# Performance work log

Hardware: AMD Instinct MI355X
Metric: run time of the kernel (lower is better)

Reference implementation:

```python
import jax, jax.numpy as jnp
import numpy as np

T, N, F_IN, H1, H2, F_OUT = 48, 4096, 64, 64, 32, 64

def setup_inputs() -> dict:
    key = jax.random.key(0)
    ks = jax.random.split(key, 14)
    sc = 0.05
    x = jax.random.normal(ks[0], (T, N, F_IN), jnp.float32)
    adj = jax.random.uniform(ks[1], (N, N), jnp.float32) / N  # roughly row-normalized dense adjacency
    fc_w = jax.random.normal(ks[2], (F_IN, H1), jnp.float32) * sc
    fc_b = jnp.zeros((H1,), jnp.float32)
    Wz = jax.random.normal(ks[3], (H1, F_OUT), jnp.float32) * sc
    Wr = jax.random.normal(ks[4], (H1, F_OUT), jnp.float32) * sc
    Wh = jax.random.normal(ks[5], (H1, F_OUT), jnp.float32) * sc
    Lz = jax.random.normal(ks[6], (2 * F_OUT, F_OUT), jnp.float32) * sc
    Lr = jax.random.normal(ks[7], (2 * F_OUT, F_OUT), jnp.float32) * sc
    Lh = jax.random.normal(ks[8], (2 * F_OUT, F_OUT), jnp.float32) * sc
    bz = jnp.zeros((F_OUT,), jnp.float32)
    br = jnp.zeros((F_OUT,), jnp.float32)
    bh = jnp.zeros((F_OUT,), jnp.float32)
    return {"x": x, "adj": adj, "fc_w": fc_w, "fc_b": fc_b,
            "Wz": Wz, "Wr": Wr, "Wh": Wh,
            "Lz": Lz, "Lr": Lr, "Lh": Lh,
            "bz": bz, "br": br, "bh": bh}

def reference(x, adj, fc_w, fc_b, Wz, Wr, Wh, Lz, Lr, Lh, bz, br, bh):
    # relu(fc(x)) followed by relu(unsqueeze) == single relu
    xh = jax.nn.relu(x @ fc_w + fc_b)          # [T, N, H1]
    h0 = jnp.zeros((N, F_OUT), x.dtype)

    def step(h, xi):
        # TGCN cell: dense graph conv A @ (X W) feeding GRU-style gates
        az = adj @ (xi @ Wz)                   # [N, F_OUT]
        ar = adj @ (xi @ Wr)
        ah = adj @ (xi @ Wh)
        z = jax.nn.sigmoid(jnp.concatenate([az, h], axis=-1) @ Lz + bz)
        r = jax.nn.sigmoid(jnp.concatenate([ar, h], axis=-1) @ Lr + br)
        h_tilde = jnp.tanh(jnp.concatenate([ah, h * r], axis=-1) @ Lh + bh)
        h_new = z * h + (1.0 - z) * h_tilde
        return h_new, None

    h, _ = jax.lax.scan(step, h0, xh)
    return h[None]                              # [1, N, F_OUT]
```

## Files before the change

kernel.cpp:

```cpp
#include <hip/hip_runtime.h>

typedef unsigned short u16;
typedef unsigned char u8;
typedef short s16x8 __attribute__((ext_vector_type(8)));
typedef unsigned short u16x4 __attribute__((ext_vector_type(4)));
typedef float f32x4 __attribute__((ext_vector_type(4)));
typedef int i32x4 __attribute__((ext_vector_type(4)));
typedef int i32x8 __attribute__((ext_vector_type(8)));

#define AS1 __attribute__((address_space(1)))
#define AS3 __attribute__((address_space(3)))

__device__ __forceinline__ void g2l16(const void* g, void* l) {
  __builtin_amdgcn_global_load_lds((const AS1 void*)g, (AS3 void*)l, 16, 0, 0);
}

__device__ __forceinline__ float b2f(u16 u) {
  union { unsigned int i; float f; } x; x.i = ((unsigned int)u) << 16; return x.f;
}
__device__ __forceinline__ u16 f2b(float f) {
  unsigned int u = __builtin_bit_cast(unsigned int, f);
  return (u16)((u + 0x7fffu + ((u >> 16) & 1u)) >> 16);
}
__device__ __forceinline__ u8 f2e4m3(float v) {
  int p = __builtin_amdgcn_cvt_pk_fp8_f32(v, 0.f, 0, false);
  return (u8)(p & 0xff);
}
__device__ __forceinline__ float sigm(float x) { return 1.f / (1.f + __expf(-x)); }
__device__ __forceinline__ float tanh_f(float x) { return 2.f / (1.f + __expf(-2.f * x)) - 1.f; }


__global__ __launch_bounds__(256) void kpre(
    const float* __restrict__ a, u8* __restrict__ ab,
    const float* __restrict__ fcw, const float* __restrict__ fcb,
    const float* __restrict__ x, u8* __restrict__ xht,
    const float* __restrict__ Wz, const float* __restrict__ Wr, const float* __restrict__ Wh,
    const float* __restrict__ Lz, const float* __restrict__ Lr, const float* __restrict__ Lh,
    u16* __restrict__ wct, u16* __restrict__ lbt) {
  int b = blockIdx.x, tid = threadIdx.x;
  if (b < 4096) {
    size_t idx = (size_t)b * 256 + tid;
    const float4* src = (const float4*)a;
    unsigned int* dst = (unsigned int*)ab;
#pragma unroll
    for (int k = 0; k < 4; ++k) {
      size_t f = idx + (size_t)k * 1048576;
      float4 v = src[f];
      unsigned int p = __builtin_amdgcn_cvt_pk_fp8_f32(v.x * 4096.f, v.y * 4096.f, 0, false);
      p = __builtin_amdgcn_cvt_pk_fp8_f32(v.z * 4096.f, v.w * 4096.f, p, true);
      int row = (int)(f >> 10);
      int col0 = ((int)f & 1023) << 2;
      unsigned int dstb = (unsigned int)(((row >> 7) * 32 + (col0 >> 7)) << 14) +
                          (((row >> 4) & 7) << 11) +
                          (((row & 15) | (((col0 >> 5) & 3) << 4)) << 5) + (col0 & 31);
      dst[dstb >> 2] = p;
    }
    return;
  }
  if (b < 4144) {
    int idx = (b - 4096) * 256 + tid;
    int c_cat = idx >> 6, hh = idx & 63;
    int g = c_cat >> 6, c = c_cat & 63;
    const float* W = (g == 0) ? Wz : (g == 1) ? Wr : Wh;
    const float* L = (g == 0) ? Lz : (g == 1) ? Lr : Lh;
    float acc = 0.f;
    for (int m = 0; m < 64; ++m) acc += W[hh * 64 + m] * L[m * 64 + c];
    wct[c_cat * 64 + hh] = f2b(acc);
    return;
  }
  if (b < 4147) {
    int g = b - 4144;
    const float* L = (g == 0) ? Lz : (g == 1) ? Lr : Lh;
    for (int i = 0; i < 16; ++i) {
      int idx = tid * 16 + i; int c = idx >> 6, hh = idx & 63;
      lbt[g * 4096 + c * 64 + hh] = f2b(L[(64 + hh) * 64 + c]);
    }
    return;
  }
  int kb = b - 4147;
  int t = kb >> 5, n0 = (kb & 31) * 128;
  __shared__ __align__(16) u16 xs[128 * 72];
  __shared__ __align__(16) u16 fw[64 * 72];
  __shared__ __align__(16) u8 xh8[64 * 128];
  __shared__ float fb[64];
  int w = tid >> 6, l = tid & 63;
#pragma unroll
  for (int i = 0; i < 16; ++i) {
    int idx = tid + i * 256;
    int h = idx & 63, f = idx >> 6;
    fw[h * 72 + f] = f2b(fcw[f * 64 + h]);
  }
  const float4* xg = (const float4*)(x + ((size_t)t * 4096 + n0) * 64);
#pragma unroll
  for (int i = 0; i < 8; ++i) {
    int f = tid + i * 256;
    float4 v = xg[f];
    u16x4 p; p[0] = f2b(v.x); p[1] = f2b(v.y); p[2] = f2b(v.z); p[3] = f2b(v.w);
    *(u16x4*)&xs[(f >> 4) * 72 + (f & 15) * 4] = p;
  }
  if (tid < 64) fb[tid] = fcb[tid];
  __syncthreads();

  int lm = l & 15, q = l >> 4;
  f32x4 acc[4][2];
#pragma unroll
  for (int i = 0; i < 4; ++i)
#pragma unroll
    for (int j = 0; j < 2; ++j)
#pragma unroll
      for (int r = 0; r < 4; ++r) acc[i][j][r] = 0.f;
#pragma unroll
  for (int s = 0; s < 2; ++s) {
    s16x8 af[4], bf[2];
#pragma unroll
    for (int i = 0; i < 4; ++i) af[i] = *(const s16x8*)&fw[(16 * i + lm) * 72 + 32 * s + q * 8];
#pragma unroll
    for (int j = 0; j < 2; ++j) bf[j] = *(const s16x8*)&xs[(32 * w + 16 * j + lm) * 72 + 32 * s + q * 8];
#pragma unroll
    for (int i = 0; i < 4; ++i)
#pragma unroll
      for (int j = 0; j < 2; ++j)
        acc[i][j] = __builtin_amdgcn_mfma_f32_16x16x32_bf16(af[i], bf[j], acc[i][j], 0, 0, 0);
  }
#pragma unroll
  for (int i = 0; i < 4; ++i)
#pragma unroll
    for (int j = 0; j < 2; ++j) {
      int node = 32 * w + 16 * j + lm;
      int h0 = 16 * i + q * 4;
#pragma unroll
      for (int r = 0; r < 4; ++r) {
        float v = acc[i][j][r] + fb[h0 + r];
        xh8[(h0 + r) * 128 + node] = f2e4m3(v > 0.f ? v : 0.f);
      }
    }
  __syncthreads();
  {
    int h = tid >> 2, seg = tid & 3;
    u8* dst = xht + (size_t)(t * 64 + h) * 4096 + n0 + seg * 32;
    const u8* src = &xh8[h * 128 + seg * 32];
    *(i32x4*)dst = *(const i32x4*)src;
    *(i32x4*)(dst + 16) = *(const i32x4*)(src + 16);
  }
}

__global__ __launch_bounds__(256) void k2(
    const u8* __restrict__ A, const u8* __restrict__ B, u16* __restrict__ M) {
  __shared__ __align__(16) u8 sh[49152];
  int tid = threadIdx.x, w = tid >> 6, l = tid & 63;
  int nt = blockIdx.x, mt = blockIdx.y;
  const u8* Bb = B + (size_t)nt * 192 * 4096;
  int lm = l & 15, q = l >> 4;
  int wm = w >> 1, wn = w & 1;
  int srow = l >> 3, scol = l & 7;
  const u8* At = A + (size_t)mt * 32 * 16384 + (size_t)(4 * wm) * 2048 + (size_t)l * 32;
  f32x4 acc[4][6];
#pragma unroll
  for (int i = 0; i < 4; ++i)
#pragma unroll
    for (int j = 0; j < 6; ++j)
#pragma unroll
      for (int r = 0; r < 4; ++r) acc[i][j][r] = 0.f;

#define STAGE_B(bsel, kk)                                                     \
  do {                                                                        \
    u8* Bs_ = sh + (bsel) * 24576;                                            \
    _Pragma("unroll") for (int j = 0; j < 6; ++j) {      \
      int r0 = 48 * w + 8 * j;                                                \
      int row = r0 + srow;                                                    \
      int c = (scol - row) & 7;                                               \
      g2l16(Bb + (size_t)row * 4096 + (kk) + c * 16, Bs_ + r0 * 128);         \
    }                                                                         \
  } while (0)

  STAGE_B(0, 0);
  __syncthreads();

  for (int it = 0; it < 32; ++it) {
    int cur = it & 1;
    i32x8 a8[4];
#pragma unroll
    for (int i = 0; i < 4; ++i)
      a8[i] = *(const i32x8*)(At + (size_t)it * 16384 + i * 2048);
    if (it < 31) STAGE_B(cur ^ 1, (it + 1) * 128);
    const u8* Bs = sh + cur * 24576;
#pragma unroll
    for (int j = 0; j < 6; ++j) {
      int rb = 96 * wn + 16 * j + lm;
      int q0 = (2 * q + rb) & 7, q1 = (2 * q + 1 + rb) & 7;
      i32x4 lo2 = *(const i32x4*)&Bs[rb * 128 + q0 * 16];
      i32x4 hi2 = *(const i32x4*)&Bs[rb * 128 + q1 * 16];
      i32x8 b8 = __builtin_shufflevector(lo2, hi2, 0, 1, 2, 3, 4, 5, 6, 7);
#pragma unroll
      for (int i = 0; i < 4; ++i)
        acc[i][j] = __builtin_amdgcn_mfma_scale_f32_16x16x128_f8f6f4(
            a8[i], b8, acc[i][j], 0, 0, 0, 127, 0, 127);
    }
    __syncthreads();
  }
#undef STAGE_B

  u16* tb = (u16*)sh;
  const float sc = 1.f / 4096.f;
#pragma unroll
  for (int p = 0; p < 2; ++p) {
    if (p) __syncthreads();
    if (wm == p) {
#pragma unroll
      for (int i = 0; i < 4; ++i)
#pragma unroll
        for (int j = 0; j < 6; ++j)
#pragma unroll
          for (int r = 0; r < 4; ++r)
            tb[(16 * i + 4 * q + r) * 200 + 96 * wn + 16 * j + lm] = f2b(acc[i][j][r] * sc);
    }
    __syncthreads();
    int row = tid >> 2, seg = tid & 3;
    u16* dst = M + (size_t)(mt * 128 + p * 64 + row) * 3072 + nt * 192 + seg * 48;
    const u16* src = &tb[row * 200 + seg * 48];
#pragma unroll
    for (int v = 0; v < 6; ++v)
      *(i32x4*)(dst + 8 * v) = *(const i32x4*)(src + 8 * v);
  }
}

__global__ __launch_bounds__(256) void k3(
    const u16* __restrict__ M, const u16* __restrict__ wct, const u16* __restrict__ lbt,
    const float* __restrict__ bz, const float* __restrict__ br, const float* __restrict__ bh,
    float* __restrict__ out) {
  __shared__ __align__(16) u16 hhi[1024], hlo[1024];
  __shared__ __align__(16) u16 rhi[1024], rlo[1024];
  int tid = threadIdx.x, w = tid >> 6, l = tid & 63;
  int nb0 = blockIdx.x * 16;
  int lm = l & 15, q = l >> 4;
  int am = lm & 7;
  int cb = 16 * w + q * 4;
  int rd0 = lm * 64 + ((q ^ am) * 8);
  int rd1 = lm * 64 + (((4 + q) ^ am) * 8);
  int wi  = lm * 64 + (((2 * w + (q >> 1)) ^ am) * 8) + 4 * (q & 1);
  s16x8 afw[3][2], afl[3][2];
#pragma unroll
  for (int g = 0; g < 3; ++g)
#pragma unroll
    for (int s = 0; s < 2; ++s) {
      afw[g][s] = *(const s16x8*)&wct[(size_t)(g * 64 + 16 * w + lm) * 64 + 32 * s + q * 8];
      afl[g][s] = *(const s16x8*)&lbt[(size_t)(g * 64 + 16 * w + lm) * 64 + 32 * s + q * 8];
    }
  for (int i = tid; i < 1024; i += 256) { hhi[i] = 0; hlo[i] = 0; }
  f32x4 bzv, brv, bhv, hv;
#pragma unroll
  for (int r = 0; r < 4; ++r) {
    bzv[r] = bz[cb + r]; brv[r] = br[cb + r]; bhv[r] = bh[cb + r]; hv[r] = 0.f;
  }
  const f32x4 zf = {0.f, 0.f, 0.f, 0.f};
  __syncthreads();

  const u16* Mrow = M + (size_t)(nb0 + lm) * 3072;
  s16x8 Mn[2];
  Mn[0] = *(const s16x8*)&Mrow[q * 8];
  Mn[1] = *(const s16x8*)&Mrow[32 + q * 8];
  f32x4 uzwC = __builtin_amdgcn_mfma_f32_16x16x32_bf16(afw[0][0], Mn[0], bzv, 0, 0, 0);
  uzwC = __builtin_amdgcn_mfma_f32_16x16x32_bf16(afw[0][1], Mn[1], uzwC, 0, 0, 0);
  f32x4 urwC = __builtin_amdgcn_mfma_f32_16x16x32_bf16(afw[1][0], Mn[0], brv, 0, 0, 0);
  urwC = __builtin_amdgcn_mfma_f32_16x16x32_bf16(afw[1][1], Mn[1], urwC, 0, 0, 0);
  f32x4 uhwC = __builtin_amdgcn_mfma_f32_16x16x32_bf16(afw[2][0], Mn[0], bhv, 0, 0, 0);
  uhwC = __builtin_amdgcn_mfma_f32_16x16x32_bf16(afw[2][1], Mn[1], uhwC, 0, 0, 0);

  for (int t = 0; t < 48; ++t) {
    if (t < 47) {
      Mn[0] = *(const s16x8*)&Mrow[(t + 1) * 64 + q * 8];
      Mn[1] = *(const s16x8*)&Mrow[(t + 1) * 64 + 32 + q * 8];
    }
    s16x8 hh0 = *(const s16x8*)&hhi[rd0], hh1 = *(const s16x8*)&hhi[rd1];
    s16x8 hl0 = *(const s16x8*)&hlo[rd0], hl1 = *(const s16x8*)&hlo[rd1];
    f32x4 uzA = __builtin_amdgcn_mfma_f32_16x16x32_bf16(afl[0][0], hh0, uzwC, 0, 0, 0);
    uzA = __builtin_amdgcn_mfma_f32_16x16x32_bf16(afl[0][1], hh1, uzA, 0, 0, 0);
    f32x4 uzB = __builtin_amdgcn_mfma_f32_16x16x32_bf16(afl[0][0], hl0, zf, 0, 0, 0);
    uzB = __builtin_amdgcn_mfma_f32_16x16x32_bf16(afl[0][1], hl1, uzB, 0, 0, 0);
    f32x4 urA = __builtin_amdgcn_mfma_f32_16x16x32_bf16(afl[1][0], hh0, urwC, 0, 0, 0);
    urA = __builtin_amdgcn_mfma_f32_16x16x32_bf16(afl[1][1], hh1, urA, 0, 0, 0);
    f32x4 urB = __builtin_amdgcn_mfma_f32_16x16x32_bf16(afl[1][0], hl0, zf, 0, 0, 0);
    urB = __builtin_amdgcn_mfma_f32_16x16x32_bf16(afl[1][1], hl1, urB, 0, 0, 0);
    f32x4 zv, rv;
#pragma unroll
    for (int r = 0; r < 4; ++r) {
      zv[r] = sigm(uzA[r] + uzB[r]);
      rv[r] = sigm(urA[r] + urB[r]);
    }
    {
      u16x4 phi, plo;
#pragma unroll
      for (int r = 0; r < 4; ++r) {
        float p = hv[r] * rv[r];
        u16 hi = f2b(p); phi[r] = hi; plo[r] = f2b(p - b2f(hi));
      }
      *(u16x4*)&rhi[wi] = phi;
      *(u16x4*)&rlo[wi] = plo;
    }
    __syncthreads();
    s16x8 rh0 = *(const s16x8*)&rhi[rd0], rh1 = *(const s16x8*)&rhi[rd1];
    s16x8 rl0 = *(const s16x8*)&rlo[rd0], rl1 = *(const s16x8*)&rlo[rd1];
    f32x4 uhA = __builtin_amdgcn_mfma_f32_16x16x32_bf16(afl[2][0], rh0, uhwC, 0, 0, 0);
    uhA = __builtin_amdgcn_mfma_f32_16x16x32_bf16(afl[2][1], rh1, uhA, 0, 0, 0);
    f32x4 uhB = __builtin_amdgcn_mfma_f32_16x16x32_bf16(afl[2][0], rl0, zf, 0, 0, 0);
    uhB = __builtin_amdgcn_mfma_f32_16x16x32_bf16(afl[2][1], rl1, uhB, 0, 0, 0);
    {
      u16x4 phi, plo;
#pragma unroll
      for (int r = 0; r < 4; ++r) {
        float th = tanh_f(uhA[r] + uhB[r]);
        float hn = zv[r] * hv[r] + (1.f - zv[r]) * th;
        hv[r] = hn;
        u16 hi = f2b(hn); phi[r] = hi; plo[r] = f2b(hn - b2f(hi));
      }
      *(u16x4*)&hhi[wi] = phi;
      *(u16x4*)&hlo[wi] = plo;
    }
    if (t < 47) {
      uzwC = __builtin_amdgcn_mfma_f32_16x16x32_bf16(afw[0][0], Mn[0], bzv, 0, 0, 0);
      uzwC = __builtin_amdgcn_mfma_f32_16x16x32_bf16(afw[0][1], Mn[1], uzwC, 0, 0, 0);
      urwC = __builtin_amdgcn_mfma_f32_16x16x32_bf16(afw[1][0], Mn[0], brv, 0, 0, 0);
      urwC = __builtin_amdgcn_mfma_f32_16x16x32_bf16(afw[1][1], Mn[1], urwC, 0, 0, 0);
      uhwC = __builtin_amdgcn_mfma_f32_16x16x32_bf16(afw[2][0], Mn[0], bhv, 0, 0, 0);
      uhwC = __builtin_amdgcn_mfma_f32_16x16x32_bf16(afw[2][1], Mn[1], uhwC, 0, 0, 0);
    }
    __syncthreads();
  }
#pragma unroll
  for (int r = 0; r < 4; ++r)
    out[(size_t)(nb0 + lm) * 64 + cb + r] = hv[r];
}

extern "C" void kernel_launch(void* const* d_in, const int* in_sizes, int n_in,
                              void* d_out, int out_size, void* d_ws, size_t ws_size,
                              hipStream_t stream) {
  const float* x   = (const float*)d_in[0];
  const float* adj = (const float*)d_in[1];
  const float* fcw = (const float*)d_in[2];
  const float* fcb = (const float*)d_in[3];
  const float* Wz  = (const float*)d_in[4];
  const float* Wr  = (const float*)d_in[5];
  const float* Wh  = (const float*)d_in[6];
  const float* Lz  = (const float*)d_in[7];
  const float* Lr  = (const float*)d_in[8];
  const float* Lh  = (const float*)d_in[9];
  const float* bz  = (const float*)d_in[10];
  const float* br  = (const float*)d_in[11];
  const float* bh  = (const float*)d_in[12];
  char* ws = (char*)d_ws;
  u8*  xht  = (u8*)(ws);
  u8*  adj8 = (u8*)(ws + (size_t)12582912);
  u16* Mm   = (u16*)(ws + (size_t)29360128);
  u16* wct  = (u16*)(ws + (size_t)54525952);
  u16* lbt  = (u16*)(ws + (size_t)54550528);
  float* outp = (float*)d_out;

  hipLaunchKernelGGL(kpre, dim3(5683), dim3(256), 0, stream,
                     adj, adj8, fcw, fcb, x, xht, Wz, Wr, Wh, Lz, Lr, Lh, wct, lbt);
  hipLaunchKernelGGL(k2, dim3(16, 32), dim3(256), 0, stream, adj8, xht, Mm);
  hipLaunchKernelGGL(k3, dim3(256), dim3(256), 0, stream, Mm, wct, lbt, bz, br, bh, outp);
}
```

Before: 257.8 us.

## Double k2 block to 512 threads and software-pipeline A/B loads with MFMA

The adjacency GEMM kernel now uses 512-thread blocks covering 256 rows, so each staged B tile in LDS is shared by twice as many waves, and the grid is halved. The main loop is manually unrolled by two with ping-pong A register buffers. B staging and the next A loads are interleaved between two halves of the MFMA work, using explicit vmcnt waits, raw barriers and s_setprio to overlap memory with matrix math. The cost is higher register pressure from the doubled A fragments, and the hand-placed waitcnt/barrier ordering is fragile.

```diff
diff --git a/kernel.cpp b/kernel.cpp
--- a/kernel.cpp
+++ b/kernel.cpp
@@ -144,7 +144,7 @@
   }
 }
 
-__global__ __launch_bounds__(256) void k2(
+__global__ __launch_bounds__(512, 2) void k2(
     const u8* __restrict__ A, const u8* __restrict__ B, u16* __restrict__ M) {
   __shared__ __align__(16) u8 sh[49152];
   int tid = threadIdx.x, w = tid >> 6, l = tid & 63;
@@ -153,7 +153,8 @@
   int lm = l & 15, q = l >> 4;
   int wm = w >> 1, wn = w & 1;
   int srow = l >> 3, scol = l & 7;
-  const u8* At = A + (size_t)mt * 32 * 16384 + (size_t)(4 * wm) * 2048 + (size_t)l * 32;
+  const u8* At = A + ((size_t)(2 * mt + (wm >> 1)) * 32) * 16384 +
+                 (size_t)(4 * (wm & 1)) * 2048 + (size_t)l * 32;
   f32x4 acc[4][6];
 #pragma unroll
   for (int i = 0; i < 4; ++i)
@@ -162,48 +163,75 @@
 #pragma unroll
       for (int r = 0; r < 4; ++r) acc[i][j][r] = 0.f;
 
-#define STAGE_B(bsel, kk)                                                     \
+#define STG(bsel, kk, j)                                                      \
   do {                                                                        \
-    u8* Bs_ = sh + (bsel) * 24576;                                            \
-    _Pragma("unroll") for (int j = 0; j < 6; ++j) {      \
-      int r0 = 48 * w + 8 * j;                                                \
-      int row = r0 + srow;                                                    \
-      int c = (scol - row) & 7;                                               \
-      g2l16(Bb + (size_t)row * 4096 + (kk) + c * 16, Bs_ + r0 * 128);         \
+    int r0 = 24 * w + 8 * (j);                                                \
+    int row = r0 + srow;                                                      \
+    int c = (scol - row) & 7;                                                 \
+    g2l16(Bb + (size_t)row * 4096 + (kk) + c * 16,                            \
+          sh + (bsel) * 24576 + r0 * 128);                                    \
+  } while (0)
+
+#define RDB(bfr, Bs, j)                                                       \
+  do {                                                                        \
+    int rb = 96 * wn + 16 * (j) + lm;                                         \
+    int q0 = (2 * q + rb) & 7, q1 = (2 * q + 1 + rb) & 7;                     \
+    i32x4 lo = *(const i32x4*)&(Bs)[rb * 128 + q0 * 16];                      \
+    i32x4 hi = *(const i32x4*)&(Bs)[rb * 128 + q1 * 16];                      \
+    bfr = __builtin_shufflevector(lo, hi, 0, 1, 2, 3, 4, 5, 6, 7);            \
+  } while (0)
+
+#define K2ITER(IT, ACUR, ANEXT)                                               \
+  do {                                                                        \
+    int cur = (IT) & 1;                                                       \
+    asm volatile("s_waitcnt vmcnt(4)" ::: "memory");       \
+    __builtin_amdgcn_s_barrier();                                             \
+    const u8* Bs = sh + cur * 24576;                                          \
+    i32x8 bfr[3];                                                             \
+                                                         \
+    RDB(bfr[0], Bs, 0); RDB(bfr[1], Bs, 1); RDB(bfr[2], Bs, 2);               \
+    if ((IT) < 31) { STG(cur ^ 1, ((IT) + 1) * 128, 0);                       \
+                     STG(cur ^ 1, ((IT) + 1) * 128, 1); }                     \
+    __builtin_amdgcn_s_setprio(1);                                            \
+    _Pragma("unroll") for (int jj = 0; jj < 3; ++jj)                          \
+      _Pragma("unroll") for (int i = 0; i < 4; ++i)                           \
+        acc[i][jj] = __builtin_amdgcn_mfma_scale_f32_16x16x128_f8f6f4(        \
+            ACUR[i], bfr[jj], acc[i][jj], 0, 0, 0, 127, 0, 127);              \
+    __builtin_amdgcn_s_setprio(0);                                            \
+                                                         \
+    RDB(bfr[0], Bs, 3); RDB(bfr[1], Bs, 4); RDB(bfr[2], Bs, 5);               \
+    if ((IT) < 31) {                                                          \
+      STG(cur ^ 1, ((IT) + 1) * 128, 2);                                      \
+      _Pragma("unroll") for (int i = 0; i < 4; ++i)                           \
+        ANEXT[i] = *(const i32x8*)(At + (size_t)((IT) + 1) * 16384 + i * 2048); \
     }                                                                         \
+    __builtin_amdgcn_s_setprio(1);                                            \
+    _Pragma("unroll") for (int jj = 0; jj < 3; ++jj)                          \
+      _Pragma("unroll") for (int i = 0; i < 4; ++i)                           \
+        acc[i][jj + 3] = __builtin_amdgcn_mfma_scale_f32_16x16x128_f8f6f4(    \
+            ACUR[i], bfr[jj], acc[i][jj + 3], 0, 0, 0, 127, 0, 127);          \
+    __builtin_amdgcn_s_setprio(0);                                            \
+    asm volatile("s_waitcnt lgkmcnt(0)" ::: "memory"); \
   } while (0)
 
-  STAGE_B(0, 0);
+  STG(0, 0, 0); STG(0, 0, 1); STG(0, 0, 2);
+  i32x8 a8A[4], a8B[4];
+#pragma unroll
+  for (int i = 0; i < 4; ++i) a8A[i] = *(const i32x8*)(At + i * 2048);
+
+  for (int itp = 0; itp < 16; ++itp) {
+    K2ITER(2 * itp, a8A, a8B);
+    K2ITER(2 * itp + 1, a8B, a8A);
+  }
+#undef K2ITER
+#undef RDB
+#undef STG
+
   __syncthreads();
-
-  for (int it = 0; it < 32; ++it) {
-    int cur = it & 1;
-    i32x8 a8[4];
-#pragma unroll
-    for (int i = 0; i < 4; ++i)
-      a8[i] = *(const i32x8*)(At + (size_t)it * 16384 + i * 2048);
-    if (it < 31) STAGE_B(cur ^ 1, (it + 1) * 128);
-    const u8* Bs = sh + cur * 24576;
-#pragma unroll
-    for (int j = 0; j < 6; ++j) {
-      int rb = 96 * wn + 16 * j + lm;
-      int q0 = (2 * q + rb) & 7, q1 = (2 * q + 1 + rb) & 7;
-      i32x4 lo2 = *(const i32x4*)&Bs[rb * 128 + q0 * 16];
-      i32x4 hi2 = *(const i32x4*)&Bs[rb * 128 + q1 * 16];
-      i32x8 b8 = __builtin_shufflevector(lo2, hi2, 0, 1, 2, 3, 4, 5, 6, 7);
-#pragma unroll
-      for (int i = 0; i < 4; ++i)
-        acc[i][j] = __builtin_amdgcn_mfma_scale_f32_16x16x128_f8f6f4(
-            a8[i], b8, acc[i][j], 0, 0, 0, 127, 0, 127);
-    }
-    __syncthreads();
-  }
-#undef STAGE_B
-
   u16* tb = (u16*)sh;
   const float sc = 1.f / 4096.f;
 #pragma unroll
-  for (int p = 0; p < 2; ++p) {
+  for (int p = 0; p < 4; ++p) {
     if (p) __syncthreads();
     if (wm == p) {
 #pragma unroll
@@ -215,11 +243,11 @@
             tb[(16 * i + 4 * q + r) * 200 + 96 * wn + 16 * j + lm] = f2b(acc[i][j][r] * sc);
     }
     __syncthreads();
-    int row = tid >> 2, seg = tid & 3;
-    u16* dst = M + (size_t)(mt * 128 + p * 64 + row) * 3072 + nt * 192 + seg * 48;
-    const u16* src = &tb[row * 200 + seg * 48];
-#pragma unroll
-    for (int v = 0; v < 6; ++v)
+    int row = tid >> 3, seg = tid & 7;
+    u16* dst = M + (size_t)(mt * 256 + p * 64 + row) * 3072 + nt * 192 + seg * 24;
+    const u16* src = &tb[row * 200 + seg * 24];
+#pragma unroll
+    for (int v = 0; v < 3; ++v)
       *(i32x4*)(dst + 8 * v) = *(const i32x4*)(src + 8 * v);
   }
 }
@@ -357,6 +385,6 @@
 
   hipLaunchKernelGGL(kpre, dim3(5683), dim3(256), 0, stream,
                      adj, adj8, fcw, fcb, x, xht, Wz, Wr, Wh, Lz, Lr, Lh, wct, lbt);
-  hipLaunchKernelGGL(k2, dim3(16, 32), dim3(256), 0, stream, adj8, xht, Mm);
+  hipLaunchKernelGGL(k2, dim3(16, 16), dim3(512), 0, stream, adj8, xht, Mm);
   hipLaunchKernelGGL(k3, dim3(256), dim3(256), 0, stream, Mm, wct, lbt, bz, br, bh, outp);
 }
```

Measured after the change: 261.7 us. About the same (+1.5%).
